# Performance work log

Hardware: AMD Instinct MI355X
Metric: run time of the kernel (lower is better)

Reference implementation:

```python
import jax, jax.numpy as jnp
import numpy as np

# config constants (from init_kwargs)
IMG_W = 800
IMG_H = 320
NUM_POINTS = 72
N_STRIPS = NUM_POINTS - 1
MAX_LANES = 4
REFINE_LAYERS = 3
CLS_W, REG_W, IOU_W = 2.0, 0.5, 2.0
ALPHA_NEG, ALPHA_POS, GAMMA = 0.1, 0.9, 2.0
LIOU_LEN = 15.0


def setup_inputs() -> dict:
    key = jax.random.key(0)
    k1, k2, k3, k4 = jax.random.split(key, 4)
    S, B, N, L, D = REFINE_LAYERS, 32, 2000, MAX_LANES, 2 + 4 + NUM_POINTS
    pred_fir = jax.random.uniform(k1, (S, B, N, D), dtype=jnp.float32)
    pred_sec = jax.random.uniform(k2, (S, B, N, D), dtype=jnp.float32)
    gt = jax.random.uniform(k3, (B, L, D), dtype=jnp.float32)
    gt = gt.at[..., 1].set(1.0)                    # all lanes valid
    # target offsets live in pixel coords; let some fall outside [0, IMG_W) to exercise invalid mask
    gt = gt.at[..., 6:].set(gt[..., 6:] * (IMG_W * 1.1) - 0.05 * IMG_W)
    diff = jax.random.uniform(k4, (S, N), dtype=jnp.float32)
    return {"predictions_fir": pred_fir, "predictions_sec": pred_sec,
            "gt_lane": gt, "diff": diff}


def _greedy_assign(cost):
    # cost: [N, L] -> matched prior row per target column, greedy without replacement
    N = cost.shape[0]
    def body(used, col):
        c = jnp.where(used, jnp.inf, col)
        r = jnp.argmin(c)
        return used.at[r].set(True), r
    _, rows = jax.lax.scan(body, jnp.zeros((N,), bool), cost.T)
    return rows  # [L] int32


def _assign_all(preds, gt):
    # preds: [S,B,N,D], gt: [B,L,D]; matching is under no_grad in the original
    p = jax.lax.stop_gradient(preds)
    t = jax.lax.stop_gradient(gt)
    score = jax.nn.softmax(p[..., :2], axis=-1)[..., 1]            # [S,B,N]
    geo = jnp.abs(p[..., :, None, 2:6] - t[None, :, None, :, 2:6]).sum(-1)   # [S,B,N,L]
    off = jnp.abs(p[..., :, None, 6:] - t[None, :, None, :, 6:] / (IMG_W - 1)).mean(-1)
    cost = geo + off - score[..., None]                            # [S,B,N,L]
    S, B, N, L = cost.shape
    rows = jax.vmap(_greedy_assign)(cost.reshape(S * B, N, L))
    return rows.reshape(S, B, L)


def _smooth_l1(d):
    ad = jnp.abs(d)
    return jnp.where(ad < 1.0, 0.5 * d * d, ad - 0.5)


def _branch_loss(preds, gt):
    # preds: [S,B,N,D], gt: [B,L,D] -> instance loss [N], last matched rows [L]
    S, B, N, _ = preds.shape
    L = gt.shape[1]
    rows = _assign_all(preds, gt)                                  # [S,B,L]

    # focal cls loss, per prior, summed over stages & batch
    cls_t = jax.nn.one_hot(rows, N, dtype=preds.dtype).sum(2)      # [S,B,N] 0/1
    logp = jax.nn.log_softmax(preds[..., :2], axis=-1)
    logpt = jnp.where(cls_t > 0, logp[..., 1], logp[..., 0])
    pt = jnp.exp(logpt)
    alpha_t = jnp.where(cls_t > 0, ALPHA_POS, ALPHA_NEG)
    cls_loss = (-alpha_t * (1.0 - pt) ** GAMMA * logpt).sum((0, 1)) / (B * REFINE_LAYERS)  # [N]

    # gather matched priors: [S,B,L,D]
    pm = jnp.take_along_axis(preds, rows[..., None], axis=2)
    tgt = gt[None]                                                 # [1,B,L,D]

    # smooth-L1 on (y, x, theta, length)
    sc = jnp.array([N_STRIPS, IMG_W - 1, 180.0, N_STRIPS], preds.dtype)
    d = pm[..., 2:6] * sc - tgt[..., 2:6] * sc
    reg_loss = (_smooth_l1(d).mean(-1) / L).sum((0, 1)) / (B * REFINE_LAYERS)  # [L]

    # line IoU loss on offsets
    rp = pm[..., 6:] * (IMG_W - 1)
    rt = jnp.broadcast_to(tgt[..., 6:], rp.shape)
    invalid = (rt < 0) | (rt >= IMG_W)
    ovr = jnp.minimum(rp + LIOU_LEN, rt + LIOU_LEN) - jnp.maximum(rp - LIOU_LEN, rt - LIOU_LEN)
    uni = jnp.maximum(rp + LIOU_LEN, rt + LIOU_LEN) - jnp.minimum(rp - LIOU_LEN, rt - LIOU_LEN)
    ovr = jnp.where(invalid, 0.0, ovr)
    uni = jnp.where(invalid, 0.0, uni)
    iou = ovr.sum(-1) / (uni.sum(-1) + 1e-9)                       # [S,B,L]
    iou_loss = ((1.0 - iou) / L).sum((0, 1)) / (B * REFINE_LAYERS) # [L]

    inst = cls_loss * CLS_W
    rows_last = rows[-1, -1]                                       # last stage, last image
    inst = inst.at[rows_last].add(reg_loss * REG_W + iou_loss * IOU_W)
    return inst


def reference(predictions_fir, predictions_sec, gt_lane, diff):
    loss_A = _branch_loss(predictions_fir, gt_lane)   # [N]
    loss_B = _branch_loss(predictions_sec, gt_lane)   # [N]
    diff_mean = diff.mean(0)                          # [N]
    delta = jax.lax.stop_gradient(jnp.median(loss_A - loss_B))
    loss_A = loss_A - delta / 2
    loss_B = loss_B + delta / 2
    total = jnp.sum((1.0 - diff_mean) * loss_A + diff_mean * loss_B)
    return total
```

## Files before the change

kernel.cpp:

```cpp
#include <hip/hip_runtime.h>
#include <math.h>

#define SDIM 3
#define BDIM 32
#define NPRI 2000
#define LDIM 4
#define DDIM 78
#define NOFF 72
#define NSB (SDIM * BDIM)
#define CHUNK 128
#define NCHUNK 16


__global__ __launch_bounds__(256) void prep_kernel(
    const float* __restrict__ gt, float* __restrict__ tgdiv,
    float* __restrict__ clsSum, float* __restrict__ corrws,
    float* __restrict__ regacc)
{
    int tid = blockIdx.x * 256 + threadIdx.x;
    if (tid < BDIM * 36 * 8) {
        int b = tid / 288, r = tid % 288, jj = r / 8, t = r % 8;
        int l = t >> 1, k = t & 1;
        tgdiv[tid] = gt[((size_t)b * LDIM + l) * DDIM + 6 + 2 * jj + k] / 799.0f;
    }
    if (tid < 2 * NPRI) { clsSum[tid] = 0.0f; corrws[tid] = 0.0f; }
    if (tid < 16) regacc[tid] = 0.0f;
}

__global__ __launch_bounds__(256) void cost_kernel(
    const float* __restrict__ predsA, const float* __restrict__ predsB,
    const float* __restrict__ gt, const float* __restrict__ tgdiv,
    float* __restrict__ costws, float* __restrict__ clsSum)
{
    const int chunk = blockIdx.x;
    const int sb = blockIdx.y;
    const int branch = blockIdx.z;
    const float* preds = branch ? predsB : predsA;
    const int bimg = sb % BDIM;
    const int tid = threadIdx.x;
    const int base_n = chunk * CHUNK;
    const int ntile = min(CHUNK, NPRI - base_n);

    __shared__ float tile[CHUNK * DDIM];

    {
        const float4* src = (const float4*)(preds + ((size_t)sb * NPRI + base_n) * DDIM);
        float4* dst = (float4*)tile;
        const int nf4 = ntile * DDIM / 4;
        for (int k = tid; k < nf4; k += 256) dst[k] = src[k];
    }
    __syncthreads();

    const int wv = tid >> 6, lane = tid & 63;
    const int i = wv * 32 + (lane >> 1);
    const int h = lane & 1;
    if (i >= ntile) return;
    const int n = base_n + i;
    const float* p = &tile[i * DDIM];

    const float* gtb = gt + (size_t)bimg * LDIM * DDIM;
    const float* tgb = tgdiv + (size_t)bimg * 288;

    float offs0 = 0.f, offs1 = 0.f, offs2 = 0.f, offs3 = 0.f;
    const int jj0 = h * 18;
#pragma unroll 6
    for (int jj = jj0; jj < jj0 + 18; ++jj) {
        float pv0 = p[6 + 2 * jj];
        float pv1 = p[7 + 2 * jj];
        const float* t8 = tgb + jj * 8;
        offs0 += fabsf(pv0 - t8[0]); offs0 += fabsf(pv1 - t8[1]);
        offs1 += fabsf(pv0 - t8[2]); offs1 += fabsf(pv1 - t8[3]);
        offs2 += fabsf(pv0 - t8[4]); offs2 += fabsf(pv1 - t8[5]);
        offs3 += fabsf(pv0 - t8[6]); offs3 += fabsf(pv1 - t8[7]);
    }
    offs0 += __shfl_xor(offs0, 1);
    offs1 += __shfl_xor(offs1, 1);
    offs2 += __shfl_xor(offs2, 1);
    offs3 += __shfl_xor(offs3, 1);

    if (h == 0) {
        float a = p[0], b1 = p[1];
        float m = fmaxf(a, b1);
        float ea = expf(a - m), eb = expf(b1 - m);
        float score = eb / (ea + eb);
        float g0 = p[2], g1 = p[3], g2 = p[4], g3 = p[5];
        float offs[4] = {offs0, offs1, offs2, offs3};
        float* cw = costws + ((size_t)(branch * NSB + sb) * LDIM) * NPRI + n;
#pragma unroll
        for (int l = 0; l < LDIM; ++l) {
            float geo = fabsf(g0 - gtb[l * DDIM + 2]) + fabsf(g1 - gtb[l * DDIM + 3])
                      + fabsf(g2 - gtb[l * DDIM + 4]) + fabsf(g3 - gtb[l * DDIM + 5]);
            cw[(size_t)l * NPRI] = geo + offs[l] / 72.0f - score;
        }
        float lse = m + logf(ea + eb);
        float logpt = a - lse;
        float pt = expf(logpt);
        float om = 1.0f - pt;
        atomicAdd(&clsSum[branch * NPRI + n], -(0.1f * om * om * logpt));
    }
}

__global__ __launch_bounds__(256) void assignloss_kernel(
    const float* __restrict__ predsA, const float* __restrict__ predsB,
    const float* __restrict__ gt, const float* __restrict__ costws,
    int* __restrict__ rowsws, float* __restrict__ regacc,
    float* __restrict__ corrws)
{
    const int sb = blockIdx.x, branch = blockIdx.y;
    const float* preds = branch ? predsB : predsA;
    const int tid = threadIdx.x;
    const int wv = tid >> 6, lane = tid & 63;
    const int bimg = sb % BDIM;

    __shared__ float cost[LDIM][NPRI];
    __shared__ float redv[4];
    __shared__ int   redi[4];
    __shared__ int   rows_lds[LDIM];

    const float4* src = (const float4*)(costws + (size_t)(branch * NSB + sb) * LDIM * NPRI);
    float4* dst = (float4*)&cost[0][0];
    for (int k = tid; k < LDIM * NPRI / 4; k += 256) dst[k] = src[k];
    __syncthreads();

    for (int l = 0; l < LDIM; ++l) {
        float bv = INFINITY; int bi = 0x7fffffff;
        for (int k = tid; k < NPRI; k += 256) {
            float v = cost[l][k];
            if (v < bv) { bv = v; bi = k; }
        }
#pragma unroll
        for (int off = 32; off > 0; off >>= 1) {
            float v2 = __shfl_down(bv, off);
            int   i2 = __shfl_down(bi, off);
            if (v2 < bv || (v2 == bv && i2 < bi)) { bv = v2; bi = i2; }
        }
        if (lane == 0) { redv[wv] = bv; redi[wv] = bi; }
        __syncthreads();
        if (tid == 0) {
            float fv = redv[0]; int fi = redi[0];
#pragma unroll
            for (int w = 1; w < 4; ++w)
                if (redv[w] < fv || (redv[w] == fv && redi[w] < fi)) { fv = redv[w]; fi = redi[w]; }
            rows_lds[l] = fi;
            cost[0][fi] = INFINITY; cost[1][fi] = INFINITY;
            cost[2][fi] = INFINITY; cost[3][fi] = INFINITY;
        }
        __syncthreads();
    }
    if (tid < LDIM && sb == NSB - 1) rowsws[branch * LDIM + tid] = rows_lds[tid];

    const int l = wv;
    const int row = rows_lds[l];
    const float* pm = preds + ((size_t)sb * NPRI + row) * DDIM;
    const float* tg = gt + ((size_t)bimg * LDIM + l) * DDIM;

    float osum = 0.f, usum = 0.f, rterm = 0.f;
    {
        float rp = pm[6 + lane] * 799.0f;
        float rt = tg[6 + lane];
        bool inv = (rt < 0.0f) || (rt >= 800.0f);
        float ov = fminf(rp, rt) - fmaxf(rp, rt) + 30.0f;
        float un = fmaxf(rp, rt) - fminf(rp, rt) + 30.0f;
        if (!inv) { osum += ov; usum += un; }
    }
    if (lane < 8) {
        float rp = pm[6 + lane + 64] * 799.0f;
        float rt = tg[6 + lane + 64];
        bool inv = (rt < 0.0f) || (rt >= 800.0f);
        float ov = fminf(rp, rt) - fmaxf(rp, rt) + 30.0f;
        float un = fmaxf(rp, rt) - fminf(rp, rt) + 30.0f;
        if (!inv) { osum += ov; usum += un; }
    }
    if (lane < 4) {
        const float scv[4] = {71.0f, 799.0f, 180.0f, 71.0f};
        float s = scv[lane];
        float d = pm[2 + lane] * s - tg[2 + lane] * s;
        float ad = fabsf(d);
        rterm = (ad < 1.0f) ? 0.5f * d * d : ad - 0.5f;
    }
#pragma unroll
    for (int off = 32; off > 0; off >>= 1) {
        osum += __shfl_down(osum, off);
        usum += __shfl_down(usum, off);
        rterm += __shfl_down(rterm, off);
    }
    if (lane == 0) {
        float iou = osum / (usum + 1e-9f);
        atomicAdd(&regacc[branch * 8 + l], (rterm / 4.0f) / 4.0f);
        atomicAdd(&regacc[branch * 8 + 4 + l], (1.0f - iou) / 4.0f);

        float a = pm[0], b1 = pm[1];
        float m = fmaxf(a, b1);
        float ea = expf(a - m), eb = expf(b1 - m);
        float lse = m + logf(ea + eb);
        float lp0 = a - lse, lp1 = b1 - lse;
        float pt0 = expf(lp0), pt1 = expf(lp1);
        float om0 = 1.0f - pt0, om1 = 1.0f - pt1;
        float neg = -(0.1f * om0 * om0 * lp0);
        float pos = -(0.9f * om1 * om1 * lp1);
        atomicAdd(&corrws[branch * NPRI + row], pos - neg);
    }
}

__global__ __launch_bounds__(1024) void final_kernel(
    const float* __restrict__ clsSum, const float* __restrict__ corrws,
    const float* __restrict__ regacc, const int* __restrict__ rowsws,
    const float* __restrict__ diff, float* __restrict__ out)
{
    __shared__ float instA[NPRI];
    __shared__ float instB[NPRI];
    __shared__ float sbuf[2048];
    __shared__ float red[1024];
    const int tid = threadIdx.x;

    for (int n = tid; n < NPRI; n += 1024) {
        float ia = (clsSum[n] + corrws[n]) * (2.0f / 96.0f);
        float ib = (clsSum[NPRI + n] + corrws[NPRI + n]) * (2.0f / 96.0f);
#pragma unroll
        for (int l = 0; l < 4; ++l) {
            if (rowsws[l] == n)
                ia += (regacc[l] / 96.0f) * 0.5f + (regacc[4 + l] / 96.0f) * 2.0f;
            if (rowsws[4 + l] == n)
                ib += (regacc[8 + l] / 96.0f) * 0.5f + (regacc[12 + l] / 96.0f) * 2.0f;
        }
        instA[n] = ia; instB[n] = ib;
        sbuf[n] = ia - ib;
    }
    if (tid < 2048 - NPRI) sbuf[NPRI + tid] = INFINITY;
    __syncthreads();

    for (int k = 2; k <= 2048; k <<= 1) {
        for (int j = k >> 1; j > 0; j >>= 1) {
            for (int i = tid; i < 2048; i += 1024) {
                int ixj = i ^ j;
                if (ixj > i) {
                    bool up = ((i & k) == 0);
                    float x = sbuf[i], y = sbuf[ixj];
                    if ((x > y) == up) { sbuf[i] = y; sbuf[ixj] = x; }
                }
            }
            __syncthreads();
        }
    }
    float delta = 0.5f * (sbuf[999] + sbuf[1000]);

    float acc = 0.0f;
    for (int n = tid; n < NPRI; n += 1024) {
        float dm = (diff[n] + diff[NPRI + n] + diff[2 * NPRI + n]) / 3.0f;
        acc += (1.0f - dm) * (instA[n] - 0.5f * delta)
             + dm * (instB[n] + 0.5f * delta);
    }
    red[tid] = acc;
    __syncthreads();
    for (int s = 512; s > 0; s >>= 1) {
        if (tid < s) red[tid] += red[tid + s];
        __syncthreads();
    }
    if (tid == 0) out[0] = red[0];
}

extern "C" void kernel_launch(void* const* d_in, const int* in_sizes, int n_in,
                              void* d_out, int out_size, void* d_ws, size_t ws_size,
                              hipStream_t stream)
{
    const float* predsA = (const float*)d_in[0];
    const float* predsB = (const float*)d_in[1];
    const float* gt     = (const float*)d_in[2];
    const float* diff   = (const float*)d_in[3];
    float* out = (float*)d_out;

    float* costws = (float*)d_ws;
    float* tgdiv  = costws + 2 * NSB * LDIM * NPRI;
    int*   rowsws = (int*)(tgdiv + BDIM * 36 * 8);
    float* clsSum = (float*)(rowsws + 8);
    float* corrws = clsSum + 2 * NPRI;
    float* regacc = corrws + 2 * NPRI;

    prep_kernel<<<40, 256, 0, stream>>>(gt, tgdiv, clsSum, corrws, regacc);

    dim3 g1(NCHUNK, NSB, 2);
    cost_kernel<<<g1, 256, 0, stream>>>(predsA, predsB, gt, tgdiv, costws, clsSum);

    dim3 g2(NSB, 2);
    assignloss_kernel<<<g2, 256, 0, stream>>>(predsA, predsB, gt, costws,
                                              rowsws, regacc, corrws);

    final_kernel<<<1, 1024, 0, stream>>>(clsSum, corrws, regacc, rowsws, diff, out);
}
```

Measured before the change: 203.3 us.

## Use direct global-to-LDS loads and 4 threads per prior in cost kernel

The cost kernel tile shrinks to 64 priors, doubling the grid size. Tile staging now uses the global_load_lds builtin instead of register-staged float4 copies. Each prior is split across 4 lanes, with a two-step shuffle reduction, and each lane writes the cost for one target lane, spreading the epilogue work. The gains are more blocks, less register traffic and parallel cost stores; the costs are extra shuffles and redundant softmax work on every lane.

```diff
diff --git a/kernel.cpp b/kernel.cpp
--- a/kernel.cpp
+++ b/kernel.cpp
@@ -8,8 +8,8 @@
 #define DDIM 78
 #define NOFF 72
 #define NSB (SDIM * BDIM)
-#define CHUNK 128
-#define NCHUNK 16
+#define CHUNK 64
+#define NCHUNK 32
 
 
 __global__ __launch_bounds__(256) void prep_kernel(
@@ -45,26 +45,30 @@
 
     {
         const float4* src = (const float4*)(preds + ((size_t)sb * NPRI + base_n) * DDIM);
-        float4* dst = (float4*)tile;
         const int nf4 = ntile * DDIM / 4;
-        for (int k = tid; k < nf4; k += 256) dst[k] = src[k];
+        for (int k = tid; k < nf4; k += 256) {
+            __builtin_amdgcn_global_load_lds(
+                (const __attribute__((address_space(1))) unsigned int*)(src + k),
+                (__attribute__((address_space(3))) unsigned int*)(&tile[k * 4]),
+                16, 0, 0);
+        }
     }
     __syncthreads();
 
     const int wv = tid >> 6, lane = tid & 63;
-    const int i = wv * 32 + (lane >> 1);
-    const int h = lane & 1;
-    if (i >= ntile) return;
-    const int n = base_n + i;
-    const float* p = &tile[i * DDIM];
+    const int il = wv * 16 + (lane >> 2);
+    const int h = lane & 3;
+    if (il >= ntile) return;
+    const int n = base_n + il;
+    const float* p = &tile[il * DDIM];
 
     const float* gtb = gt + (size_t)bimg * LDIM * DDIM;
     const float* tgb = tgdiv + (size_t)bimg * 288;
 
     float offs0 = 0.f, offs1 = 0.f, offs2 = 0.f, offs3 = 0.f;
-    const int jj0 = h * 18;
-#pragma unroll 6
-    for (int jj = jj0; jj < jj0 + 18; ++jj) {
+    const int jj0 = h * 9;
+#pragma unroll 3
+    for (int jj = jj0; jj < jj0 + 9; ++jj) {
         float pv0 = p[6 + 2 * jj];
         float pv1 = p[7 + 2 * jj];
         const float* t8 = tgb + jj * 8;
@@ -73,25 +77,27 @@
         offs2 += fabsf(pv0 - t8[4]); offs2 += fabsf(pv1 - t8[5]);
         offs3 += fabsf(pv0 - t8[6]); offs3 += fabsf(pv1 - t8[7]);
     }
-    offs0 += __shfl_xor(offs0, 1);
-    offs1 += __shfl_xor(offs1, 1);
-    offs2 += __shfl_xor(offs2, 1);
-    offs3 += __shfl_xor(offs3, 1);
+    offs0 += __shfl_xor(offs0, 1); offs1 += __shfl_xor(offs1, 1);
+    offs2 += __shfl_xor(offs2, 1); offs3 += __shfl_xor(offs3, 1);
+    offs0 += __shfl_xor(offs0, 2); offs1 += __shfl_xor(offs1, 2);
+    offs2 += __shfl_xor(offs2, 2); offs3 += __shfl_xor(offs3, 2);
+
+    float a = p[0], b1 = p[1];
+    float m = fmaxf(a, b1);
+    float ea = expf(a - m), eb = expf(b1 - m);
+    float score = eb / (ea + eb);
+    float g0 = p[2], g1 = p[3], g2 = p[4], g3 = p[5];
+
+    float mo01 = (h & 1) ? offs1 : offs0;
+    float mo23 = (h & 1) ? offs3 : offs2;
+    float myoffs = (h & 2) ? mo23 : mo01;
+
+    float geo = fabsf(g0 - gtb[h * DDIM + 2]) + fabsf(g1 - gtb[h * DDIM + 3])
+              + fabsf(g2 - gtb[h * DDIM + 4]) + fabsf(g3 - gtb[h * DDIM + 5]);
+    float* cw = costws + ((size_t)(branch * NSB + sb) * LDIM) * NPRI;
+    cw[(size_t)h * NPRI + n] = geo + myoffs / 72.0f - score;
 
     if (h == 0) {
-        float a = p[0], b1 = p[1];
-        float m = fmaxf(a, b1);
-        float ea = expf(a - m), eb = expf(b1 - m);
-        float score = eb / (ea + eb);
-        float g0 = p[2], g1 = p[3], g2 = p[4], g3 = p[5];
-        float offs[4] = {offs0, offs1, offs2, offs3};
-        float* cw = costws + ((size_t)(branch * NSB + sb) * LDIM) * NPRI + n;
-#pragma unroll
-        for (int l = 0; l < LDIM; ++l) {
-            float geo = fabsf(g0 - gtb[l * DDIM + 2]) + fabsf(g1 - gtb[l * DDIM + 3])
-                      + fabsf(g2 - gtb[l * DDIM + 4]) + fabsf(g3 - gtb[l * DDIM + 5]);
-            cw[(size_t)l * NPRI] = geo + offs[l] / 72.0f - score;
-        }
         float lse = m + logf(ea + eb);
         float logpt = a - lse;
         float pt = expf(logpt);
```

Measured after the change: 198.2 us. -2.5%, faster.
